# Kernel optimization log

Measured on AMD Instinct MI355X. Metric: run time of the kernel, lower is better.

The kernel has to match this reference:

```python
import jax, jax.numpy as jnp
import numpy as np

B, N, E, H = 4, 2048, 768, 8
D = E // H
SCALING = D ** (-0.5)


def setup_inputs() -> dict:
    key = jax.random.key(0)
    k0, k1, k2, k3, k4 = jax.random.split(key, 5)
    x = jax.random.normal(k0, (B, N, E), dtype=jnp.float32)
    Wqkv = jax.random.normal(k1, (E, 3 * E), dtype=jnp.float32) * 0.02
    bqkv = jax.random.normal(k2, (3 * E,), dtype=jnp.float32) * 0.02
    Wproj = jax.random.normal(k3, (E, E), dtype=jnp.float32) * 0.02
    bproj = jax.random.normal(k4, (E,), dtype=jnp.float32) * 0.02
    return {"x": x, "Wqkv": Wqkv, "bqkv": bqkv, "Wproj": Wproj, "bproj": bproj}


def reference(x, Wqkv, bqkv, Wproj, bproj):
    b, n, e = x.shape
    h, d = H, E // H
    # QKV projection: [b, n, 3e]
    qkv = x @ Wqkv + bqkv
    # rearrange 'b n (h d qkv) -> qkv b h n d': qkv is the INNERMOST axis
    qkv = qkv.reshape(b, n, h, d, 3)
    q = jnp.transpose(qkv[..., 0], (0, 2, 1, 3))  # [b, h, n, d]
    k = jnp.transpose(qkv[..., 1], (0, 2, 1, 3))
    v = jnp.transpose(qkv[..., 2], (0, 2, 1, 3))
    # unscaled attention scores, softmax, then post-softmax scaling (as in source)
    energy = jnp.einsum('bhqd,bhkd->bhqk', q, k)  # [b, h, n, n]
    att = jax.nn.softmax(energy, axis=-1) * SCALING
    out = jnp.einsum('bhqk,bhkd->bhqd', att, v)   # [b, h, n, d]
    out = jnp.transpose(out, (0, 2, 1, 3)).reshape(b, n, e)
    return out @ Wproj + bproj
```

## Files before the change

### kernel.cpp

```cpp
#include <hip/hip_runtime.h>
#include <cstdint>

#define BB 4
#define SEQ 2048
#define EMB 768
#define NH 8
#define HD 96
#define E3 2304
#define MTOK 8192
#define NROWS 65536
#define KSPLIT 4
#define SCALING 0.10206207261596575f
#define LOG2E 1.44269504f

typedef unsigned short u16;
typedef unsigned int u32;
typedef __bf16 bf16x8 __attribute__((ext_vector_type(8)));
typedef float f32x4 __attribute__((ext_vector_type(4)));
typedef float f32x16 __attribute__((ext_vector_type(16)));

__device__ __forceinline__ u16 f2bf(float f) {
    union { float f; uint32_t u; } c; c.f = f;
    uint32_t u = c.u;
    return (u16)((u + 0x7FFFu + ((u >> 16) & 1u)) >> 16);
}
__device__ __forceinline__ u16 f2bf_fast(float f) {
    union { float f; uint32_t u; } c; c.f = f;
    return (u16)((c.u + 0x8000u) >> 16);
}
__device__ __forceinline__ uint32_t pk2(float a, float b) {
    return (uint32_t)f2bf(a) | ((uint32_t)f2bf(b) << 16);
}
__device__ __forceinline__ uint32_t pk2_fast(float a, float b) {
    return (uint32_t)f2bf_fast(a) | ((uint32_t)f2bf_fast(b) << 16);
}
__device__ __forceinline__ float bf2f(u16 h) {
    union { uint32_t u; float f; } c; c.u = ((uint32_t)h) << 16; return c.f;
}
__device__ __forceinline__ float fexp2(float x) {
    return __builtin_amdgcn_exp2f(x);
}
__device__ __forceinline__ void async16(const u16* g, u16* l) {
    __builtin_amdgcn_global_load_lds(
        (const __attribute__((address_space(1))) void*)g,
        (__attribute__((address_space(3))) void*)l, 16, 0, 0);
}


__device__ __forceinline__ void transpose_body(const float* __restrict__ src,
                                               u16* __restrict__ dst,
                                               int ncols, int mode, int j0, int k0,
                                               int tid, float (*T)[65]) {
#pragma unroll
    for (int it = 0; it < 16; ++it) {
        int lin = it * 256 + tid;
        int rr2 = lin >> 6, jj = lin & 63;
        int j = j0 + jj;
        int c;
        if (mode == 0) c = j;
        else if (mode == 1) { int s = j / 768, rr = j % 768; c = (rr / 96) * 288 + (rr % 96) * 3 + s; }
        else { c = (j / 96) * 288 + (j % 96) * 3 + 2; }
        T[rr2][jj] = src[(k0 + rr2) * ncols + c];
    }
    __syncthreads();
#pragma unroll
    for (int it = 0; it < 16; ++it) {
        int lin = it * 256 + tid;
        int jr = lin >> 6, kc = lin & 63;
        dst[(size_t)(j0 + jr) * 768 + k0 + kc] = f2bf(T[kc][jr]);
    }
}

__global__ __launch_bounds__(256) void prep_kernel(const float* __restrict__ x,
                                                   const float* __restrict__ Wqkv,
                                                   const float* __restrict__ Wproj,
                                                   u16* __restrict__ xb,
                                                   u16* __restrict__ wqkT,
                                                   u16* __restrict__ wvr,
                                                   u16* __restrict__ wpt) {
    __shared__ float T[64][65];
    int bid = blockIdx.x, tid = threadIdx.x;
    if (bid < 3072) {
        int i = bid * 256 + tid;
        const float4* s4 = (const float4*)x;
        float4 a = s4[2 * i];
        float4 c = s4[2 * i + 1];
        uint4 o;
        o.x = pk2(a.x, a.y); o.y = pk2(a.z, a.w);
        o.z = pk2(c.x, c.y); o.w = pk2(c.z, c.w);
        ((uint4*)xb)[i] = o;
    } else if (bid < 3360) {
        int t = bid - 3072;
        transpose_body(Wqkv, wqkT, E3, 1, (t % 24) * 64, (t / 24) * 64, tid, T);
    } else if (bid < 3504) {
        int t = bid - 3360;
        transpose_body(Wqkv, wvr, E3, 2, (t % 12) * 64, (t / 12) * 64, tid, T);
    } else {
        int t = bid - 3504;
        transpose_body(Wproj, wpt, EMB, 0, (t % 12) * 64, (t / 12) * 64, tid, T);
    }
}


__device__ __forceinline__ void gemm_tiles(const u16* __restrict__ A,
                                           const u16* __restrict__ Bt,
                                           int m0, int n0, int tid,
                                           u16* As, u16* Bs, f32x4 acc[4][4]) {
    const int lane = tid & 63;
    const int w = tid >> 6;
    const int l15 = lane & 15;
    const int quad = lane >> 4;
    const int wr = (w >> 1) * 64;
    const int wc = (w & 1) * 64;
    const int swz = l15 & 7;
    for (int kb = 0; kb < 768; kb += 64) {
#pragma unroll
        for (int it = 0; it < 4; ++it) {
            int base = (w * 4 + it) * 64;
            int lin = base + lane;
            int row = lin >> 3, cl = lin & 7;
            int cg = cl ^ (row & 7);
            async16(&A[(size_t)(m0 + row) * 768 + kb + cg * 8], &As[base * 8]);
            async16(&Bt[(size_t)(n0 + row) * 768 + kb + cg * 8], &Bs[base * 8]);
        }
        __syncthreads();
#pragma unroll
        for (int ks = 0; ks < 2; ++ks) {
            bf16x8 af[4], bfg[4];
#pragma unroll
            for (int fi = 0; fi < 4; ++fi)
                af[fi] = *(const bf16x8*)&As[(wr + fi * 16 + l15) * 64 + (((ks * 4 + quad) ^ swz) * 8)];
#pragma unroll
            for (int fj = 0; fj < 4; ++fj)
                bfg[fj] = *(const bf16x8*)&Bs[(wc + fj * 16 + l15) * 64 + (((ks * 4 + quad) ^ swz) * 8)];
#pragma unroll
            for (int fi = 0; fi < 4; ++fi)
#pragma unroll
                for (int fj = 0; fj < 4; ++fj)
                    acc[fi][fj] = __builtin_amdgcn_mfma_f32_16x16x32_bf16(af[fi], bfg[fj], acc[fi][fj], 0, 0, 0);
        }
        __syncthreads();
    }
}

__device__ __forceinline__ void gemm_tiles64(const u16* __restrict__ A,
                                             const u16* __restrict__ Bt,
                                             int m0, int n0, int tid,
                                             u16* As, u16* Bs, f32x4 acc[4][2]) {
    const int lane = tid & 63;
    const int w = tid >> 6;
    const int l15 = lane & 15;
    const int quad = lane >> 4;
    const int wr = (w >> 1) * 64;
    const int wc = (w & 1) * 32;
    const int swz = l15 & 7;
    for (int kb = 0; kb < 768; kb += 64) {
#pragma unroll
        for (int it = 0; it < 4; ++it) {
            int base = (w * 4 + it) * 64;
            int lin = base + lane;
            int row = lin >> 3, cl = lin & 7;
            int cg = cl ^ (row & 7);
            async16(&A[(size_t)(m0 + row) * 768 + kb + cg * 8], &As[base * 8]);
        }
#pragma unroll
        for (int it = 0; it < 2; ++it) {
            int base = (w * 2 + it) * 64;
            int lin = base + lane;
            int row = lin >> 3, cl = lin & 7;
            int cg = cl ^ (row & 7);
            async16(&Bt[(size_t)(n0 + row) * 768 + kb + cg * 8], &Bs[base * 8]);
        }
        __syncthreads();
#pragma unroll
        for (int ks = 0; ks < 2; ++ks) {
            bf16x8 af[4], bfg[2];
#pragma unroll
            for (int fi = 0; fi < 4; ++fi)
                af[fi] = *(const bf16x8*)&As[(wr + fi * 16 + l15) * 64 + (((ks * 4 + quad) ^ swz) * 8)];
#pragma unroll
            for (int fj = 0; fj < 2; ++fj)
                bfg[fj] = *(const bf16x8*)&Bs[(wc + fj * 16 + l15) * 64 + (((ks * 4 + quad) ^ swz) * 8)];
#pragma unroll
            for (int fi = 0; fi < 4; ++fi)
#pragma unroll
                for (int fj = 0; fj < 2; ++fj)
                    acc[fi][fj] = __builtin_amdgcn_mfma_f32_16x16x32_bf16(af[fi], bfg[fj], acc[fi][fj], 0, 0, 0);
        }
        __syncthreads();
    }
}

__global__ __launch_bounds__(256) void gemm_qk_kernel(const u16* __restrict__ A,
                                                      const u16* __restrict__ Bt,
                                                      const float* __restrict__ bqkv,
                                                      u16* __restrict__ qb,
                                                      u16* __restrict__ kg) {
    __shared__ __align__(16) u16 As[128 * 64];
    __shared__ __align__(16) u16 Bs[128 * 64];
    int tid = threadIdx.x;
    int n0 = blockIdx.x * 128, m0 = blockIdx.y * 128;
    f32x4 acc[4][4] = {};
    gemm_tiles(A, Bt, m0, n0, tid, As, Bs, acc);
    int lane = tid & 63, w = tid >> 6, l15 = lane & 15, quad = lane >> 4;
    int wr = (w >> 1) * 64, wc = (w & 1) * 64;
#pragma unroll
    for (int fj = 0; fj < 4; ++fj) {
        int j = n0 + wc + fj * 16 + l15;
        int s = j / 768, rr = j % 768;
        int hh = rr / 96, dd = rr % 96;
        float bv = bqkv[hh * 288 + dd * 3 + s];
#pragma unroll
        for (int fi = 0; fi < 4; ++fi) {
#pragma unroll
            for (int r = 0; r < 4; ++r) {
                int m = m0 + wr + fi * 16 + quad * 4 + r;
                int b = m >> 11, n = m & 2047;
                int bh = b * NH + hh;
                float v = acc[fi][fj][r] + bv;
                if (s == 0) {
                    qb[((size_t)bh * SEQ + n) * HD + dd] = f2bf(v * LOG2E);
                } else {
                    int cp = (dd >> 3) ^ (n & 7);
                    kg[((size_t)bh * SEQ + n) * 128 + cp * 8 + (dd & 7)] = f2bf(v);
                }
            }
        }
    }
}

__global__ __launch_bounds__(256) void gemm_v_kernel(const u16* __restrict__ A,
                                                     const u16* __restrict__ Bt,
                                                     const float* __restrict__ bqkv,
                                                     u16* __restrict__ vt) {
    __shared__ __align__(16) u16 As[128 * 64];
    __shared__ __align__(16) u16 Bs[64 * 64];
    int tid = threadIdx.x;
    int n0 = blockIdx.x * 64, m0 = blockIdx.y * 128;
    f32x4 acc[4][2] = {};
    gemm_tiles64(A, Bt, m0, n0, tid, As, Bs, acc);
    int lane = tid & 63, w = tid >> 6, l15 = lane & 15, quad = lane >> 4;
    int wr = (w >> 1) * 64, wc = (w & 1) * 32;
    float bvs[4][4]; int hhs[4][4], dds[4][4];
#pragma unroll
    for (int fi = 0; fi < 4; ++fi)
#pragma unroll
        for (int r = 0; r < 4; ++r) {
            int m = m0 + wr + fi * 16 + quad * 4 + r;
            int hh = m / 96, dd = m % 96;
            hhs[fi][r] = hh; dds[fi][r] = dd;
            bvs[fi][r] = bqkv[hh * 288 + dd * 3 + 2];
        }
#pragma unroll
    for (int fj = 0; fj < 2; ++fj) {
        int n = n0 + wc + fj * 16 + l15;
        int b = n >> 11, nn = n & 2047;
#pragma unroll
        for (int fi = 0; fi < 4; ++fi) {
#pragma unroll
            for (int r = 0; r < 4; ++r) {
                int dd = dds[fi][r];
                int kk = (nn & ~63) | ((((nn >> 3) ^ dd) & 7) << 3) | (nn & 7);
                vt[((size_t)(b * NH + hhs[fi][r]) * HD + dd) * SEQ + kk] =
                    f2bf(acc[fi][fj][r] + bvs[fi][r]);
            }
        }
    }
}

__global__ __launch_bounds__(256) void gemm_proj_kernel(const u16* __restrict__ A,
                                                        const u16* __restrict__ Bt,
                                                        const float* __restrict__ bias,
                                                        float* __restrict__ out) {
    __shared__ __align__(16) u16 As[128 * 64];
    __shared__ __align__(16) u16 Bs[64 * 64];
    int tid = threadIdx.x;
    int n0 = blockIdx.x * 64, m0 = blockIdx.y * 128;
    f32x4 acc[4][2] = {};
    gemm_tiles64(A, Bt, m0, n0, tid, As, Bs, acc);
    int lane = tid & 63, w = tid >> 6, l15 = lane & 15, quad = lane >> 4;
    int wr = (w >> 1) * 64, wc = (w & 1) * 32;
#pragma unroll
    for (int fj = 0; fj < 2; ++fj) {
        int j = n0 + wc + fj * 16 + l15;
        float bv = bias[j];
#pragma unroll
        for (int fi = 0; fi < 4; ++fi) {
#pragma unroll
            for (int r = 0; r < 4; ++r) {
                int m = m0 + wr + fi * 16 + quad * 4 + r;
                out[(size_t)m * 768 + j] = acc[fi][fj][r] + bv;
            }
        }
    }
}

__global__ __launch_bounds__(256, 2) void attn_kernel(const u16* __restrict__ Q,
                                                      const u16* __restrict__ Kg,
                                                      const u16* __restrict__ Vt,
                                                      u16* __restrict__ part,
                                                      float* __restrict__ lpart) {
    __shared__ __align__(16) u16 Ks[64 * 128];
    __shared__ __align__(16) u16 Vs[96 * 64];
    int tid = threadIdx.x;
    int lane = tid & 63, w = tid >> 6;
    int l31 = lane & 31, hf = lane >> 5;
    int swz = l31 & 7;
    int bid = blockIdx.x;
    int qt = bid >> 7;
    int g = bid & 127;
    int bh = g >> 2, kh = g & 3;
    const u16* qp = Q + (size_t)bh * SEQ * HD;
    const u16* kgp = Kg + (size_t)bh * SEQ * 128;
    const u16* vtp = Vt + (size_t)bh * HD * SEQ;
    int qbase = qt * 256 + w * 64;
    int kbase = kh * 512;

    bf16x8 aq[2][6];
#pragma unroll
    for (int j = 0; j < 2; ++j)
#pragma unroll
        for (int dc = 0; dc < 6; ++dc)
            aq[j][dc] = *(const bf16x8*)&qp[(size_t)(qbase + j * 32 + l31) * HD + dc * 16 + hf * 8];

    f32x16 Ot[2][3] = {};
    float lp[2] = {0.f, 0.f};

    for (int kt = 0; kt < 8; ++kt) {
        int k0 = kbase + kt * 64;
#pragma unroll
        for (int it = 0; it < 4; ++it) {
            int cw = w * 4 + it;
            async16(kgp + (size_t)(k0 + cw * 4 + (lane >> 4)) * 128 + (lane & 15) * 8,
                    &Ks[cw * 512]);
        }
#pragma unroll
        for (int it = 0; it < 3; ++it) {
            int vw = w * 3 + it;
            async16(vtp + (size_t)(vw * 8 + (lane >> 3)) * SEQ + k0 + (lane & 7) * 8,
                    &Vs[vw * 512]);
        }
        __syncthreads();

#pragma unroll
        for (int tau = 0; tau < 2; ++tau) {
            f32x16 Sv0 = {}, Sv1 = {};
#pragma unroll
            for (int dc = 0; dc < 6; ++dc) {
                bf16x8 ka = *(const bf16x8*)&Ks[(tau * 32 + l31) * 128 + (((2 * dc + hf) ^ swz) * 8)];
                Sv0 = __builtin_amdgcn_mfma_f32_32x32x16_bf16(ka, aq[0][dc], Sv0, 0, 0, 0);
                Sv1 = __builtin_amdgcn_mfma_f32_32x32x16_bf16(ka, aq[1][dc], Sv1, 0, 0, 0);
            }
            u32 pk[2][4][2];
#pragma unroll
            for (int g2 = 0; g2 < 4; ++g2)
#pragma unroll
                for (int u = 0; u < 2; ++u) {
                    float a0 = fexp2(Sv0[g2 * 4 + 2 * u]);
                    float a1 = fexp2(Sv0[g2 * 4 + 2 * u + 1]);
                    lp[0] += a0 + a1;
                    pk[0][g2][u] = pk2_fast(a0, a1);
                    float b0 = fexp2(Sv1[g2 * 4 + 2 * u]);
                    float b1 = fexp2(Sv1[g2 * 4 + 2 * u + 1]);
                    lp[1] += b0 + b1;
                    pk[1][g2][u] = pk2_fast(b0, b1);
                }
            u32 rv[2][2][2];
#pragma unroll
            for (int j = 0; j < 2; ++j)
#pragma unroll
                for (int kc = 0; kc < 2; ++kc)
#pragma unroll
                    for (int u = 0; u < 2; ++u) {
                        u32 send = hf ? pk[j][2 * kc][u] : pk[j][2 * kc + 1][u];
                        rv[j][kc][u] = (u32)__shfl_xor((int)send, 32);
                    }
#pragma unroll
            for (int kc = 0; kc < 2; ++kc) {
                union { u32 u[4]; bf16x8 v; } pf0, pf1;
                pf0.u[0] = hf ? rv[0][kc][0] : pk[0][2 * kc][0];
                pf0.u[1] = hf ? rv[0][kc][1] : pk[0][2 * kc][1];
                pf0.u[2] = hf ? pk[0][2 * kc + 1][0] : rv[0][kc][0];
                pf0.u[3] = hf ? pk[0][2 * kc + 1][1] : rv[0][kc][1];
                pf1.u[0] = hf ? rv[1][kc][0] : pk[1][2 * kc][0];
                pf1.u[1] = hf ? rv[1][kc][1] : pk[1][2 * kc][1];
                pf1.u[2] = hf ? pk[1][2 * kc + 1][0] : rv[1][kc][0];
                pf1.u[3] = hf ? pk[1][2 * kc + 1][1] : rv[1][kc][1];
#pragma unroll
                for (int t = 0; t < 3; ++t) {
                    bf16x8 va = *(const bf16x8*)&Vs[(t * 32 + l31) * 64 + (((4 * tau + 2 * kc + hf) ^ swz) * 8)];
                    Ot[0][t] = __builtin_amdgcn_mfma_f32_32x32x16_bf16(va, pf0.v, Ot[0][t], 0, 0, 0);
                    Ot[1][t] = __builtin_amdgcn_mfma_f32_32x32x16_bf16(va, pf1.v, Ot[1][t], 0, 0, 0);
                }
            }
        }
        __syncthreads();
    }

    size_t pb = (size_t)kh * NROWS + (size_t)bh * SEQ;
#pragma unroll
    for (int j = 0; j < 2; ++j) {
        int q = qbase + j * 32 + l31;
        float lr = lp[j] + __shfl_xor(lp[j], 32);
        if (hf == 0) lpart[pb + q] = lr;
        size_t rowb = (pb + q) * HD;
#pragma unroll
        for (int t = 0; t < 3; ++t) {
#pragma unroll
            for (int g2 = 0; g2 < 4; ++g2) {
                int d0 = t * 32 + 8 * g2 + 4 * hf;
                uint2 val;
                val.x = pk2(Ot[j][t][g2 * 4 + 0], Ot[j][t][g2 * 4 + 1]);
                val.y = pk2(Ot[j][t][g2 * 4 + 2], Ot[j][t][g2 * 4 + 3]);
                *(uint2*)&part[rowb + d0] = val;
            }
        }
    }
}

__global__ __launch_bounds__(256) void combine_kernel(const u16* __restrict__ part,
                                                      const float* __restrict__ lpart,
                                                      u16* __restrict__ ao) {
    int idx = blockIdx.x * 256 + threadIdx.x;
    int row = idx / 12, ch = idx % 12;
    float l = 0.f;
#pragma unroll
    for (int k = 0; k < KSPLIT; ++k) l += lpart[(size_t)k * NROWS + row];
    float sc = SCALING / l;
    float acc[8] = {};
#pragma unroll
    for (int k = 0; k < KSPLIT; ++k) {
        uint4 pv = *(const uint4*)&part[((size_t)k * NROWS + row) * HD + ch * 8];
        const u16* a = (const u16*)&pv;
#pragma unroll
        for (int i = 0; i < 8; ++i) acc[i] += bf2f(a[i]);
    }
    uint4 o;
    u32* ou = (u32*)&o;
#pragma unroll
    for (int i = 0; i < 4; ++i)
        ou[i] = pk2(acc[2 * i] * sc, acc[2 * i + 1] * sc);
    int bh = row >> 11, n = row & 2047;
    int b = bh >> 3, h = bh & 7;
    *(uint4*)&ao[((size_t)(b * SEQ + n)) * EMB + h * HD + ch * 8] = o;
}


extern "C" void kernel_launch(void* const* d_in, const int* in_sizes, int n_in,
                              void* d_out, int out_size, void* d_ws, size_t ws_size,
                              hipStream_t stream) {
    const float* x     = (const float*)d_in[0];
    const float* Wqkv  = (const float*)d_in[1];
    const float* bqkv  = (const float*)d_in[2];
    const float* Wproj = (const float*)d_in[3];
    const float* bproj = (const float*)d_in[4];
    float* out = (float*)d_out;

    char* p = (char*)d_ws;
    u16*   qb    = (u16*)p;  p += (size_t)NROWS * HD * 2;
    u16*   kg    = (u16*)p;  p += (size_t)NROWS * 128 * 2;
    u16*   vt    = (u16*)p;  p += (size_t)NROWS * HD * 2;
    u16*   ao    = (u16*)p;  p += (size_t)MTOK * EMB * 2;
    u16*   wpt   = (u16*)p;  p += (size_t)EMB * EMB * 2;
    float* lpart = (float*)p; p += (size_t)KSPLIT * NROWS * 4;
    char*  U     = p;
    u16*   xb    = (u16*)U;
    u16*   wqkT  = (u16*)(U + (size_t)MTOK * EMB * 2);
    u16*   wvr   = (u16*)(U + (size_t)MTOK * EMB * 2 + (size_t)1536 * EMB * 2);
    u16*   partb = (u16*)U;

    prep_kernel<<<3648, 256, 0, stream>>>(x, Wqkv, Wproj, xb, wqkT, wvr, wpt);
    gemm_qk_kernel<<<dim3(1536 / 128, MTOK / 128), 256, 0, stream>>>(xb, wqkT, bqkv, qb, kg);
    gemm_v_kernel<<<dim3(MTOK / 64, EMB / 128), 256, 0, stream>>>(wvr, xb, bqkv, vt);
    attn_kernel<<<8 * 32 * KSPLIT, 256, 0, stream>>>(qb, kg, vt, partb, lpart);
    combine_kernel<<<NROWS * 12 / 256, 256, 0, stream>>>(partb, lpart, ao);
    gemm_proj_kernel<<<dim3(EMB / 64, MTOK / 128), 256, 0, stream>>>(ao, wpt, bproj, out);
}
```

Baseline: 241.4 us.

## Double-buffer K/V tiles in attention and use permlane swap and cvt_pk

```diff
diff --git a/kernel.cpp b/kernel.cpp
--- a/kernel.cpp
+++ b/kernel.cpp
@@ -24,15 +24,13 @@
     uint32_t u = c.u;
     return (u16)((u + 0x7FFFu + ((u >> 16) & 1u)) >> 16);
 }
-__device__ __forceinline__ u16 f2bf_fast(float f) {
-    union { float f; uint32_t u; } c; c.f = f;
-    return (u16)((c.u + 0x8000u) >> 16);
-}
 __device__ __forceinline__ uint32_t pk2(float a, float b) {
     return (uint32_t)f2bf(a) | ((uint32_t)f2bf(b) << 16);
 }
-__device__ __forceinline__ uint32_t pk2_fast(float a, float b) {
-    return (uint32_t)f2bf_fast(a) | ((uint32_t)f2bf_fast(b) << 16);
+__device__ __forceinline__ uint32_t cvtpk(float a, float b) {
+    uint32_t r;
+    asm("v_cvt_pk_bf16_f32 %0, %1, %2" : "=v"(r) : "v"(a), "v"(b));
+    return r;
 }
 __device__ __forceinline__ float bf2f(u16 h) {
     union { uint32_t u; float f; } c; c.u = ((uint32_t)h) << 16; return c.f;
@@ -300,8 +298,8 @@
                                                       const u16* __restrict__ Vt,
                                                       u16* __restrict__ part,
                                                       float* __restrict__ lpart) {
-    __shared__ __align__(16) u16 Ks[64 * 128];
-    __shared__ __align__(16) u16 Vs[96 * 64];
+    __shared__ __align__(16) u16 Ks[2 * 64 * 128];
+    __shared__ __align__(16) u16 Vs[2 * 96 * 64];
     int tid = threadIdx.x;
     int lane = tid & 63, w = tid >> 6;
     int l31 = lane & 31, hf = lane >> 5;
@@ -326,31 +324,37 @@
     f32x16 Ot[2][3] = {};
     float lp[2] = {0.f, 0.f};
 
-    for (int kt = 0; kt < 8; ++kt) {
+    u16* Ks0 = Ks;            u16* Ks1 = Ks + 64 * 128;
+    u16* Vs0 = Vs;            u16* Vs1 = Vs + 96 * 64;
+
+    auto STAGE = [&](int kt, u16* kdst, u16* vdst) {
         int k0 = kbase + kt * 64;
 #pragma unroll
         for (int it = 0; it < 4; ++it) {
             int cw = w * 4 + it;
             async16(kgp + (size_t)(k0 + cw * 4 + (lane >> 4)) * 128 + (lane & 15) * 8,
-                    &Ks[cw * 512]);
+                    &kdst[cw * 512]);
         }
 #pragma unroll
         for (int it = 0; it < 3; ++it) {
             int vw = w * 3 + it;
             async16(vtp + (size_t)(vw * 8 + (lane >> 3)) * SEQ + k0 + (lane & 7) * 8,
-                    &Vs[vw * 512]);
-        }
-        __syncthreads();
-
+                    &vdst[vw * 512]);
+        }
+    };
+
+    auto COMPUTE = [&](const u16* ksrc, const u16* vsrc) {
 #pragma unroll
         for (int tau = 0; tau < 2; ++tau) {
             f32x16 Sv0 = {}, Sv1 = {};
+            __builtin_amdgcn_s_setprio(1);
 #pragma unroll
             for (int dc = 0; dc < 6; ++dc) {
-                bf16x8 ka = *(const bf16x8*)&Ks[(tau * 32 + l31) * 128 + (((2 * dc + hf) ^ swz) * 8)];
+                bf16x8 ka = *(const bf16x8*)&ksrc[(tau * 32 + l31) * 128 + (((2 * dc + hf) ^ swz) * 8)];
                 Sv0 = __builtin_amdgcn_mfma_f32_32x32x16_bf16(ka, aq[0][dc], Sv0, 0, 0, 0);
                 Sv1 = __builtin_amdgcn_mfma_f32_32x32x16_bf16(ka, aq[1][dc], Sv1, 0, 0, 0);
             }
+            __builtin_amdgcn_s_setprio(0);
             u32 pk[2][4][2];
 #pragma unroll
             for (int g2 = 0; g2 < 4; ++g2)
@@ -359,41 +363,47 @@
                     float a0 = fexp2(Sv0[g2 * 4 + 2 * u]);
                     float a1 = fexp2(Sv0[g2 * 4 + 2 * u + 1]);
                     lp[0] += a0 + a1;
-                    pk[0][g2][u] = pk2_fast(a0, a1);
+                    pk[0][g2][u] = cvtpk(a0, a1);
                     float b0 = fexp2(Sv1[g2 * 4 + 2 * u]);
                     float b1 = fexp2(Sv1[g2 * 4 + 2 * u + 1]);
                     lp[1] += b0 + b1;
-                    pk[1][g2][u] = pk2_fast(b0, b1);
+                    pk[1][g2][u] = cvtpk(b0, b1);
                 }
-            u32 rv[2][2][2];
 #pragma unroll
             for (int j = 0; j < 2; ++j)
 #pragma unroll
                 for (int kc = 0; kc < 2; ++kc)
 #pragma unroll
-                    for (int u = 0; u < 2; ++u) {
-                        u32 send = hf ? pk[j][2 * kc][u] : pk[j][2 * kc + 1][u];
-                        rv[j][kc][u] = (u32)__shfl_xor((int)send, 32);
-                    }
+                    for (int u = 0; u < 2; ++u)
+                        asm("v_permlane32_swap_b32 %0, %1"
+                            : "+v"(pk[j][2 * kc][u]), "+v"(pk[j][2 * kc + 1][u]));
 #pragma unroll
             for (int kc = 0; kc < 2; ++kc) {
                 union { u32 u[4]; bf16x8 v; } pf0, pf1;
-                pf0.u[0] = hf ? rv[0][kc][0] : pk[0][2 * kc][0];
-                pf0.u[1] = hf ? rv[0][kc][1] : pk[0][2 * kc][1];
-                pf0.u[2] = hf ? pk[0][2 * kc + 1][0] : rv[0][kc][0];
-                pf0.u[3] = hf ? pk[0][2 * kc + 1][1] : rv[0][kc][1];
-                pf1.u[0] = hf ? rv[1][kc][0] : pk[1][2 * kc][0];
-                pf1.u[1] = hf ? rv[1][kc][1] : pk[1][2 * kc][1];
-                pf1.u[2] = hf ? pk[1][2 * kc + 1][0] : rv[1][kc][0];
-                pf1.u[3] = hf ? pk[1][2 * kc + 1][1] : rv[1][kc][1];
+                pf0.u[0] = pk[0][2 * kc][0];     pf0.u[1] = pk[0][2 * kc][1];
+                pf0.u[2] = pk[0][2 * kc + 1][0]; pf0.u[3] = pk[0][2 * kc + 1][1];
+                pf1.u[0] = pk[1][2 * kc][0];     pf1.u[1] = pk[1][2 * kc][1];
+                pf1.u[2] = pk[1][2 * kc + 1][0]; pf1.u[3] = pk[1][2 * kc + 1][1];
+                __builtin_amdgcn_s_setprio(1);
 #pragma unroll
                 for (int t = 0; t < 3; ++t) {
-                    bf16x8 va = *(const bf16x8*)&Vs[(t * 32 + l31) * 64 + (((4 * tau + 2 * kc + hf) ^ swz) * 8)];
+                    bf16x8 va = *(const bf16x8*)&vsrc[(t * 32 + l31) * 64 + (((4 * tau + 2 * kc + hf) ^ swz) * 8)];
                     Ot[0][t] = __builtin_amdgcn_mfma_f32_32x32x16_bf16(va, pf0.v, Ot[0][t], 0, 0, 0);
                     Ot[1][t] = __builtin_amdgcn_mfma_f32_32x32x16_bf16(va, pf1.v, Ot[1][t], 0, 0, 0);
                 }
-            }
-        }
+                __builtin_amdgcn_s_setprio(0);
+            }
+        }
+    };
+
+    STAGE(0, Ks0, Vs0);
+    __syncthreads();
+    for (int kt = 0; kt < 8; kt += 2) {
+        if (kt < 7) STAGE(kt + 1, Ks1, Vs1);
+        COMPUTE(Ks0, Vs0);
+        __syncthreads();
+        if (kt < 6) STAGE(kt + 2, Ks0, Vs0);
+        COMPUTE(Ks1, Vs1);
         __syncthreads();
     }
 
```

After: 285.9 us. +18.5%, slower.
